# Optimization experiments

Measured on AMD Instinct MI355X. Metric: run time of the kernel, lower is better.

## Reference

```python
import jax, jax.numpy as jnp
import numpy as np

B, S, D, F, E, K = 2, 2048, 1024, 1024, 8, 2


def setup_inputs() -> dict:
    key = jax.random.key(0)
    kx, kg, k1, k3, k2 = jax.random.split(key, 5)
    # kaiming_uniform_(a=sqrt(5)) => Uniform(-1/sqrt(fan_in), 1/sqrt(fan_in))
    x = jax.random.normal(kx, (B, S, D), dtype=jnp.float32)
    gate_w = jax.random.uniform(kg, (E, D), jnp.float32, -1.0, 1.0) / np.sqrt(D)
    w1 = jax.random.uniform(k1, (E, F, D), jnp.float32, -1.0, 1.0) / np.sqrt(D)
    w3 = jax.random.uniform(k3, (E, F, D), jnp.float32, -1.0, 1.0) / np.sqrt(D)
    w2 = jax.random.uniform(k2, (E, D, F), jnp.float32, -1.0, 1.0) / np.sqrt(F)
    return {"x": x, "gate_w": gate_w, "w1": w1, "w3": w3, "w2": w2}


def reference(x, gate_w, w1, w3, w2):
    b, s, d = x.shape
    T = b * s
    xf = x.reshape(T, d)                      # [T, D]
    # ---- Gate: softmax scores, top-k selection, renormalized weights ----
    logits = xf @ gate_w.T                    # [T, E]
    probs = jax.nn.softmax(logits, axis=-1)
    topk_w, topk_idx = jax.lax.top_k(probs, K)            # [T, K]
    topk_w = topk_w / jnp.sum(topk_w, axis=-1, keepdims=True)
    # Dense per-token gate matrix [T, E]; zero for unselected experts, so the
    # weighted combine below is exactly sum_k w_k * expert_{idx_k}(x).
    gate_full = jnp.zeros((T, E), x.dtype).at[
        jnp.arange(T)[:, None], topk_idx].add(topk_w)
    # ---- Grouped SwiGLU experts: loop over small fixed E, vectorized over tokens ----
    out = jnp.zeros_like(xf)
    for e in range(E):
        h = jax.nn.silu(xf @ w1[e].T) * (xf @ w3[e].T)    # [T, F]
        out = out + gate_full[:, e:e + 1] * (h @ w2[e].T)  # [T, D]
    return out.reshape(b, s, d)
```

## Files before the change

### kernel.cpp

```cpp
#include <hip/hip_runtime.h>
#include <hip/hip_bf16.h>
#include <cstdint>
#include <cstddef>

#define T_TOK 4096
#define DDIM  1024
#define FDIM  1024
#define NEXP  8

typedef __attribute__((ext_vector_type(8))) short bf16x8;
typedef __attribute__((ext_vector_type(4))) float f32x4;
typedef __attribute__((ext_vector_type(8))) unsigned short u16x8;

__device__ __forceinline__ unsigned short f2bf(float f) {
  unsigned int u = __float_as_uint(f);
  u += 0x7FFFu + ((u >> 16) & 1u);
  return (unsigned short)(u >> 16);
}
__device__ __forceinline__ float bf2f(unsigned short u) {
  return __uint_as_float(((unsigned int)u) << 16);
}

__device__ __forceinline__ void gload_lds16(const void* g, void* l) {
  __builtin_amdgcn_global_load_lds(
      (const __attribute__((address_space(1))) unsigned int*)g,
      (__attribute__((address_space(3))) unsigned int*)l, 16, 0, 0);
}

__device__ __forceinline__ void vwait6() { asm volatile("s_waitcnt vmcnt(6)" ::: "memory"); }
__device__ __forceinline__ void vwait0() { asm volatile("s_waitcnt vmcnt(0)" ::: "memory"); }
__device__ __forceinline__ void lwait0() { asm volatile("s_waitcnt lgkmcnt(0)" ::: "memory"); }
__device__ __forceinline__ void barr()   { asm volatile("s_barrier" ::: "memory"); }

__device__ __forceinline__ bf16x8 frag_ld(const unsigned short* tile, int row, int kk) {
  int byteoff = (row << 7) + ((kk * 2) ^ ((row & 7) << 4));
  return *reinterpret_cast<const bf16x8*>(reinterpret_cast<const char*>(tile) + byteoff);
}

__global__ __launch_bounds__(256) void prep_kernel(
    const float* __restrict__ w1, const float* __restrict__ w3,
    unsigned short* __restrict__ W1b, unsigned short* __restrict__ W3b,
    const float* __restrict__ x, const float* __restrict__ gw,
    unsigned int* __restrict__ Xb32, int* __restrict__ tkidx, float* __restrict__ tkw,
    int* __restrict__ curp) {
  __shared__ float gws[NEXP * DDIM];
  const int bid = blockIdx.x;
  const int tid = threadIdx.x;

  if (bid < 2048) {
    const int sub = bid >> 10;
    const int b = bid & 1023;
    const float* s = (sub == 0) ? w1 : w3;
    unsigned short* d = (sub == 0) ? W1b : W3b;
    const int n = NEXP * FDIM * DDIM;
    const int stride = 1024 * 256 * 8;
    for (int i = (b * 256 + tid) * 8; i < n; i += stride) {
      float4 a = *reinterpret_cast<const float4*>(s + i);
      float4 c = *reinterpret_cast<const float4*>(s + i + 4);
      u16x8 o;
      o[0] = f2bf(a.x); o[1] = f2bf(a.y); o[2] = f2bf(a.z); o[3] = f2bf(a.w);
      o[4] = f2bf(c.x); o[5] = f2bf(c.y); o[6] = f2bf(c.z); o[7] = f2bf(c.w);
      *reinterpret_cast<u16x8*>(d + i) = o;
    }
    return;
  }

  const int lane = tid & 63;
  const int wid = tid >> 6;
  if (bid == 2048 && tid < NEXP) curp[tid * 32] = 0;
  for (int i = tid; i < NEXP * DDIM / 4; i += 256)
    reinterpret_cast<float4*>(gws)[i] = reinterpret_cast<const float4*>(gw)[i];
  __syncthreads();

  const int t = (bid - 2048) * 4 + wid;
  const float2* xr = reinterpret_cast<const float2*>(x + (size_t)t * DDIM);
  float2 xv[8];
#pragma unroll
  for (int i = 0; i < 8; ++i) xv[i] = xr[i * 64 + lane];
#pragma unroll
  for (int i = 0; i < 8; ++i)
    Xb32[(size_t)t * 512 + i * 64 + lane] =
        (unsigned int)f2bf(xv[i].x) | ((unsigned int)f2bf(xv[i].y) << 16);
  float p[NEXP];
#pragma unroll
  for (int e = 0; e < NEXP; ++e) p[e] = 0.f;
#pragma unroll
  for (int i = 0; i < 8; ++i) {
    const int k = (i * 64 + lane) * 2;
#pragma unroll
    for (int e = 0; e < NEXP; ++e)
      p[e] += xv[i].x * gws[e * DDIM + k] + xv[i].y * gws[e * DDIM + k + 1];
  }
#pragma unroll
  for (int s = 32; s > 0; s >>= 1)
#pragma unroll
    for (int e = 0; e < NEXP; ++e) p[e] += __shfl_xor(p[e], s, 64);
  if (lane == 0) {
    int i0 = 0; float l0 = p[0];
#pragma unroll
    for (int e = 1; e < NEXP; ++e) if (p[e] > l0) { l0 = p[e]; i0 = e; }
    int i1 = -1; float l1 = -1e30f;
#pragma unroll
    for (int e = 0; e < NEXP; ++e) if (e != i0 && p[e] > l1) { l1 = p[e]; i1 = e; }
    float ex = __expf(l1 - l0);
    float w0 = 1.f / (1.f + ex);
    float w1v = ex / (1.f + ex);
    tkidx[t * 2] = i0; tkidx[t * 2 + 1] = i1;
    tkw[t * 2] = w0;   tkw[t * 2 + 1] = w1v;
  }
}

__global__ __launch_bounds__(256) void fill_kernel(const int* __restrict__ tkidx,
                                                   const float* __restrict__ tkw,
                                                   int* __restrict__ offp,
                                                   int* __restrict__ curp,
                                                   int* __restrict__ list,
                                                   float* __restrict__ rgate,
                                                   int* __restrict__ wmap,
                                                   int* __restrict__ nwp) {
  __shared__ int ghist[4][NEXP];
  __shared__ int lhist[NEXP], base[NEXP];
  const int tid = threadIdx.x;
  if (tid < 32) ghist[tid >> 3][tid & 7] = 0;
  if (tid < NEXP) lhist[tid] = 0;
  __syncthreads();
  for (int i = tid; i < 2 * T_TOK; i += 256)
    atomicAdd(&ghist[tid >> 6][tkidx[i]], 1);
  const int t = blockIdx.x * 256 + tid;
  const int e0 = tkidx[t * 2], e1 = tkidx[t * 2 + 1];
  const int r0 = atomicAdd(&lhist[e0], 1);
  const int r1 = atomicAdd(&lhist[e1], 1);
  __syncthreads();
  if (blockIdx.x == 0 && tid == 64) {
    int nw = 0;
    for (int e = 0; e < NEXP; ++e) {
      int c = ghist[0][e] + ghist[1][e] + ghist[2][e] + ghist[3][e];
      int nrt = (c + 127) >> 7;
      for (int r = 0; r < nrt; ++r) wmap[nw++] = (e << 8) | r;
    }
    nwp[0] = nw;
  }
  if (tid < NEXP) {
    int o = 0;
#pragma unroll
    for (int j = 0; j < NEXP; ++j) {
      int c = ghist[0][j] + ghist[1][j] + ghist[2][j] + ghist[3][j];
      if (j < tid) o += c;
    }
    if (blockIdx.x == 0) {
      offp[tid] = o;
      if (tid == NEXP - 1)
        offp[NEXP] = o + ghist[0][tid] + ghist[1][tid] + ghist[2][tid] + ghist[3][tid];
    }
    base[tid] = o + atomicAdd(&curp[tid * 32], lhist[tid]);
  }
  __syncthreads();
  const int p0 = base[e0] + r0;
  const int p1 = base[e1] + r1;
  list[p0] = (t << 1);     rgate[p0] = tkw[t * 2];
  list[p1] = (t << 1) | 1; rgate[p1] = tkw[t * 2 + 1];
}

__global__ __launch_bounds__(256) void gemm1_kernel(
    const unsigned short* __restrict__ Xb, const unsigned short* __restrict__ W1b,
    const unsigned short* __restrict__ W3b, unsigned short* __restrict__ Hb,
    const int* __restrict__ off, const int* __restrict__ list,
    const int* __restrict__ wmap, const int* __restrict__ nwp,
    const float* __restrict__ w2, unsigned short* __restrict__ W2b) {
  const int bid0 = blockIdx.x;
  const int tid = threadIdx.x;

  if (bid0 >= 72 * 32) {
    const int b = bid0 - 72 * 32;
    const int n = NEXP * FDIM * DDIM;
    const int stride = 1024 * 256 * 8;
    for (int i = (b * 256 + tid) * 8; i < n; i += stride) {
      float4 a = *reinterpret_cast<const float4*>(w2 + i);
      float4 c = *reinterpret_cast<const float4*>(w2 + i + 4);
      u16x8 o;
      o[0] = f2bf(a.x); o[1] = f2bf(a.y); o[2] = f2bf(a.z); o[3] = f2bf(a.w);
      o[4] = f2bf(c.x); o[5] = f2bf(c.y); o[6] = f2bf(c.z); o[7] = f2bf(c.w);
      *reinterpret_cast<u16x8*>(W2b + i) = o;
    }
    return;
  }

  const int slot = bid0 >> 5;
  const int ft = bid0 & 31;
  if (slot >= nwp[0]) return;
  const int ent = wmap[slot];
  const int e = ent >> 8;
  const int rt = ent & 255;
  const int seg0 = off[e];
  const int Ne = off[e + 1] - seg0;
  const int rowbase = rt * 128;
  const int f0 = ft * 32;

  __shared__ unsigned short As[2][128 * 64];
  __shared__ unsigned short B1s[2][32 * 64];
  __shared__ unsigned short B3s[2][32 * 64];

  const int lane = tid & 63;
  const int wid = tid >> 6;
  const int wr = wid >> 1, wc = wid & 1;

  int ldsoffA[4]; size_t abase[4];
#pragma unroll
  for (int j = 0; j < 4; ++j) {
    int boff = j * 4096 + wid * 1024 + lane * 16;
    int row = boff >> 7;
    int c = ((boff >> 4) & 7) ^ (row & 7);
    ldsoffA[j] = (j * 4096 + wid * 1024) >> 1;
    int ar = rowbase + row; if (ar > Ne - 1) ar = Ne - 1;
    int tok = list[seg0 + ar] >> 1;
    abase[j] = (size_t)tok * DDIM + c * 8;
  }
  int ldsoffB; size_t bbase;
  {
    int boff = tid * 16;
    int row = boff >> 7;
    int c = ((boff >> 4) & 7) ^ (row & 7);
    ldsoffB = (wid * 1024) >> 1;
    bbase = (size_t)(e * FDIM + f0 + row) * DDIM + c * 8;
  }

  f32x4 acc1[4], acc3[4];
  const f32x4 z = {0.f, 0.f, 0.f, 0.f};
#pragma unroll
  for (int m = 0; m < 4; ++m) { acc1[m] = z; acc3[m] = z; }

  auto stage = [&](int buf, int kt) {
    const int ko = kt * 64;
#pragma unroll
    for (int j = 0; j < 4; ++j)
      gload_lds16(Xb + abase[j] + ko, &As[buf][ldsoffA[j]]);
    gload_lds16(W1b + bbase + ko, &B1s[buf][ldsoffB]);
    gload_lds16(W3b + bbase + ko, &B3s[buf][ldsoffB]);
  };

  const int lrow = lane & 15;
  const int kb = (lane >> 4) * 8;

  vwait0();
  stage(0, 0);
  stage(1, 1);
  vwait6();
  barr();

  for (int t = 0; t < 16; ++t) {
    const int b = t & 1;
#pragma unroll
    for (int ks = 0; ks < 2; ++ks) {
      bf16x8 a[4], p, q;
#pragma unroll
      for (int m = 0; m < 4; ++m)
        a[m] = frag_ld(As[b], wr * 64 + m * 16 + lrow, ks * 32 + kb);
      p = frag_ld(B1s[b], wc * 16 + lrow, ks * 32 + kb);
      q = frag_ld(B3s[b], wc * 16 + lrow, ks * 32 + kb);
#pragma unroll
      for (int m = 0; m < 4; ++m) {
        acc1[m] = __builtin_amdgcn_mfma_f32_16x16x32_bf16(a[m], p, acc1[m], 0, 0, 0);
        acc3[m] = __builtin_amdgcn_mfma_f32_16x16x32_bf16(a[m], q, acc3[m], 0, 0, 0);
      }
    }
    if (t == 15) break;
    lwait0();
    barr();
    if (t + 2 < 16) stage(b, t + 2);
    if (t < 14) vwait6(); else vwait0();
    barr();
  }

#pragma unroll
  for (int m = 0; m < 4; ++m)
#pragma unroll
    for (int r = 0; r < 4; ++r) {
      int rloc = wr * 64 + m * 16 + ((lane >> 4) << 2) + r;
      if (rowbase + rloc < Ne) {
        float v1 = acc1[m][r], v3 = acc3[m][r];
        float h = v1 / (1.f + __expf(-v1)) * v3;
        int col = f0 + wc * 16 + (lane & 15);
        Hb[(size_t)(seg0 + rowbase + rloc) * FDIM + col] = f2bf(h);
      }
    }
}

__global__ __launch_bounds__(256) void gemm2_kernel(
    const unsigned short* __restrict__ Hb, const unsigned short* __restrict__ W2b,
    unsigned short* __restrict__ Yb, const int* __restrict__ off,
    const int* __restrict__ list, const float* __restrict__ rgate,
    const int* __restrict__ wmap, const int* __restrict__ nwp) {
  const int bid0 = blockIdx.x;
  const int slot = bid0 >> 4;
  const int dt = bid0 & 15;
  if (slot >= nwp[0]) return;
  const int ent = wmap[slot];
  const int e = ent >> 8;
  const int rt = ent & 255;
  const int seg0 = off[e];
  const int Ne = off[e + 1] - seg0;
  const int rowbase = rt * 128;
  const int d0 = dt * 64;

  __shared__ unsigned short As[2][128 * 64];
  __shared__ unsigned short Bs[2][64 * 64];

  const int tid = threadIdx.x;
  const int lane = tid & 63;
  const int wid = tid >> 6;
  const int wr = wid >> 1, wc = wid & 1;

  int ldsoffA[4]; size_t abase[4];
  int ldsoffB[2]; size_t bbase[2];
#pragma unroll
  for (int j = 0; j < 4; ++j) {
    int boff = j * 4096 + wid * 1024 + lane * 16;
    int row = boff >> 7;
    int c = ((boff >> 4) & 7) ^ (row & 7);
    ldsoffA[j] = (j * 4096 + wid * 1024) >> 1;
    int ar = rowbase + row; if (ar > Ne - 1) ar = Ne - 1;
    abase[j] = (size_t)(seg0 + ar) * FDIM + c * 8;
  }
#pragma unroll
  for (int j = 0; j < 2; ++j) {
    int boff = j * 4096 + wid * 1024 + lane * 16;
    int row = boff >> 7;
    int c = ((boff >> 4) & 7) ^ (row & 7);
    ldsoffB[j] = (j * 4096 + wid * 1024) >> 1;
    bbase[j] = (size_t)(e * DDIM + d0 + row) * FDIM + c * 8;
  }

  f32x4 acc[4][2];
  const f32x4 z = {0.f, 0.f, 0.f, 0.f};
#pragma unroll
  for (int m = 0; m < 4; ++m)
#pragma unroll
    for (int n = 0; n < 2; ++n) acc[m][n] = z;

  auto stage = [&](int buf, int kt) {
    const int ko = kt * 64;
#pragma unroll
    for (int j = 0; j < 4; ++j)
      gload_lds16(Hb + abase[j] + ko, &As[buf][ldsoffA[j]]);
#pragma unroll
    for (int j = 0; j < 2; ++j)
      gload_lds16(W2b + bbase[j] + ko, &Bs[buf][ldsoffB[j]]);
  };

  const int lrow = lane & 15;
  const int kb = (lane >> 4) * 8;

  vwait0();
  stage(0, 0);
  stage(1, 1);
  vwait6();
  barr();

  for (int t = 0; t < 16; ++t) {
    const int b = t & 1;
#pragma unroll
    for (int ks = 0; ks < 2; ++ks) {
      bf16x8 a[4], bb[2];
#pragma unroll
      for (int m = 0; m < 4; ++m)
        a[m] = frag_ld(As[b], wr * 64 + m * 16 + lrow, ks * 32 + kb);
#pragma unroll
      for (int n = 0; n < 2; ++n)
        bb[n] = frag_ld(Bs[b], wc * 32 + n * 16 + lrow, ks * 32 + kb);
#pragma unroll
      for (int m = 0; m < 4; ++m)
#pragma unroll
        for (int n = 0; n < 2; ++n)
          acc[m][n] = __builtin_amdgcn_mfma_f32_16x16x32_bf16(a[m], bb[n], acc[m][n], 0, 0, 0);
    }
    if (t == 15) break;
    lwait0();
    barr();
    if (t + 2 < 16) stage(b, t + 2);
    if (t < 14) vwait6(); else vwait0();
    barr();
  }

#pragma unroll
  for (int m = 0; m < 4; ++m)
#pragma unroll
    for (int r = 0; r < 4; ++r) {
      int rloc = wr * 64 + m * 16 + ((lane >> 4) << 2) + r;
      if (rowbase + rloc < Ne) {
        int rg = seg0 + rowbase + rloc;
        int tk = list[rg];
        float gsc = rgate[rg];
#pragma unroll
        for (int n = 0; n < 2; ++n) {
          int col = d0 + wc * 32 + n * 16 + (lane & 15);
          Yb[(size_t)tk * DDIM + col] = f2bf(gsc * acc[m][n][r]);
        }
      }
    }
}

__global__ __launch_bounds__(256) void combine_kernel(const unsigned short* __restrict__ Yb,
                                                      float* __restrict__ out) {
  const int n = T_TOK * DDIM / 8;
  const int stride = gridDim.x * blockDim.x;
  for (int i = blockIdx.x * blockDim.x + threadIdx.x; i < n; i += stride) {
    int t = i >> 7;
    int c = (i & 127) * 8;
    u16x8 a = *reinterpret_cast<const u16x8*>(Yb + ((size_t)t * 2) * DDIM + c);
    u16x8 b = *reinterpret_cast<const u16x8*>(Yb + ((size_t)t * 2 + 1) * DDIM + c);
    float4 o0, o1;
    o0.x = bf2f(a[0]) + bf2f(b[0]); o0.y = bf2f(a[1]) + bf2f(b[1]);
    o0.z = bf2f(a[2]) + bf2f(b[2]); o0.w = bf2f(a[3]) + bf2f(b[3]);
    o1.x = bf2f(a[4]) + bf2f(b[4]); o1.y = bf2f(a[5]) + bf2f(b[5]);
    o1.z = bf2f(a[6]) + bf2f(b[6]); o1.w = bf2f(a[7]) + bf2f(b[7]);
    float* dst = out + (size_t)t * DDIM + c;
    *reinterpret_cast<float4*>(dst) = o0;
    *reinterpret_cast<float4*>(dst + 4) = o1;
  }
}

extern "C" void kernel_launch(void* const* d_in, const int* in_sizes, int n_in,
                              void* d_out, int out_size, void* d_ws, size_t ws_size,
                              hipStream_t stream) {
  (void)in_sizes; (void)n_in; (void)ws_size; (void)out_size;
  const float* x  = (const float*)d_in[0];
  const float* gw = (const float*)d_in[1];
  const float* w1 = (const float*)d_in[2];
  const float* w3 = (const float*)d_in[3];
  const float* w2 = (const float*)d_in[4];
  float* out = (float*)d_out;

  char* ws = (char*)d_ws;
  unsigned short* Xb  = (unsigned short*)(ws + 0);
  unsigned short* W1b = (unsigned short*)(ws + 8388608);
  unsigned short* W3b = (unsigned short*)(ws + 25165824);
  unsigned short* W2b = (unsigned short*)(ws + 41943040);
  unsigned short* Hb  = (unsigned short*)(ws + 58720256);
  unsigned short* Yb  = (unsigned short*)(ws + 8388608);
  int*   ctrl  = (int*)(ws + 75497472);
  int*   off   = ctrl;
  int*   nwp   = ctrl + 12;
  int*   curp  = ctrl + 16;
  int*   wmap  = ctrl + 256;
  int*   tkidx = (int*)(ws + 75497472 + 4096);
  float* tkw   = (float*)(ws + 75497472 + 4096 + 32768);
  int*   list  = (int*)(ws + 75497472 + 4096 + 65536);
  float* rgate = (float*)(ws + 75497472 + 4096 + 98304);

  prep_kernel<<<3072, 256, 0, stream>>>(w1, w3, W1b, W3b,
                                        x, gw, (unsigned int*)Xb, tkidx, tkw, curp);
  fill_kernel<<<16, 256, 0, stream>>>(tkidx, tkw, off, curp, list, rgate, wmap, nwp);

  gemm1_kernel<<<72 * 32 + 1024, 256, 0, stream>>>(Xb, W1b, W3b, Hb, off, list,
                                                   wmap, nwp, w2, W2b);
  gemm2_kernel<<<72 * 16, 256, 0, stream>>>(Hb, W2b, Yb, off, list, rgate, wmap, nwp);
  combine_kernel<<<2048, 256, 0, stream>>>(Yb, out);
}
```

Baseline: 132.9 us.

## Widen gemm1 F tile to 128 and drop double-buffered async pipeline

The gemm1 tile grows from 128x32 to 128x128 in F, so each block computes 4x4 MFMA sub-tiles per wave for both W1 and W3. This cuts the grid from 2304 to 576 compute blocks and reuses each A tile across four times more columns. The two-stage LDS pipeline with explicit vmcnt waits is replaced by a single-buffered load, syncthreads, compute, syncthreads loop. That exposes global load latency, and the accumulator count rises to 128 floats per thread, which adds register pressure and lowers occupancy.

```diff
diff --git a/kernel.cpp b/kernel.cpp
--- a/kernel.cpp
+++ b/kernel.cpp
@@ -170,8 +170,8 @@
   const int bid0 = blockIdx.x;
   const int tid = threadIdx.x;
 
-  if (bid0 >= 72 * 32) {
-    const int b = bid0 - 72 * 32;
+  if (bid0 >= 72 * 8) {
+    const int b = bid0 - 72 * 8;
     const int n = NEXP * FDIM * DDIM;
     const int stride = 1024 * 256 * 8;
     for (int i = (b * 256 + tid) * 8; i < n; i += stride) {
@@ -185,8 +185,8 @@
     return;
   }
 
-  const int slot = bid0 >> 5;
-  const int ft = bid0 & 31;
+  const int slot = bid0 >> 3;
+  const int ft = bid0 & 7;
   if (slot >= nwp[0]) return;
   const int ent = wmap[slot];
   const int e = ent >> 8;
@@ -194,81 +194,65 @@
   const int seg0 = off[e];
   const int Ne = off[e + 1] - seg0;
   const int rowbase = rt * 128;
-  const int f0 = ft * 32;
-
-  __shared__ unsigned short As[2][128 * 64];
-  __shared__ unsigned short B1s[2][32 * 64];
-  __shared__ unsigned short B3s[2][32 * 64];
+  const int f0 = ft * 128;
+
+  __shared__ unsigned short As[128 * 64];
+  __shared__ unsigned short B1s[128 * 64];
+  __shared__ unsigned short B3s[128 * 64];
 
   const int lane = tid & 63;
   const int wid = tid >> 6;
   const int wr = wid >> 1, wc = wid & 1;
 
-  int ldsoffA[4]; size_t abase[4];
+  int ldsoff[4]; size_t abase[4]; size_t bbase[4];
 #pragma unroll
   for (int j = 0; j < 4; ++j) {
     int boff = j * 4096 + wid * 1024 + lane * 16;
     int row = boff >> 7;
     int c = ((boff >> 4) & 7) ^ (row & 7);
-    ldsoffA[j] = (j * 4096 + wid * 1024) >> 1;
+    ldsoff[j] = (j * 4096 + wid * 1024) >> 1;
     int ar = rowbase + row; if (ar > Ne - 1) ar = Ne - 1;
     int tok = list[seg0 + ar] >> 1;
     abase[j] = (size_t)tok * DDIM + c * 8;
-  }
-  int ldsoffB; size_t bbase;
-  {
-    int boff = tid * 16;
-    int row = boff >> 7;
-    int c = ((boff >> 4) & 7) ^ (row & 7);
-    ldsoffB = (wid * 1024) >> 1;
-    bbase = (size_t)(e * FDIM + f0 + row) * DDIM + c * 8;
-  }
-
-  f32x4 acc1[4], acc3[4];
+    bbase[j] = (size_t)(e * FDIM + f0 + row) * DDIM + c * 8;
+  }
+
+  f32x4 acc1[4][4], acc3[4][4];
   const f32x4 z = {0.f, 0.f, 0.f, 0.f};
 #pragma unroll
-  for (int m = 0; m < 4; ++m) { acc1[m] = z; acc3[m] = z; }
-
-  auto stage = [&](int buf, int kt) {
-    const int ko = kt * 64;
-#pragma unroll
-    for (int j = 0; j < 4; ++j)
-      gload_lds16(Xb + abase[j] + ko, &As[buf][ldsoffA[j]]);
-    gload_lds16(W1b + bbase + ko, &B1s[buf][ldsoffB]);
-    gload_lds16(W3b + bbase + ko, &B3s[buf][ldsoffB]);
-  };
+  for (int m = 0; m < 4; ++m)
+#pragma unroll
+    for (int n = 0; n < 4; ++n) { acc1[m][n] = z; acc3[m][n] = z; }
 
   const int lrow = lane & 15;
   const int kb = (lane >> 4) * 8;
-
-  vwait0();
-  stage(0, 0);
-  stage(1, 1);
-  vwait6();
-  barr();
-
-  for (int t = 0; t < 16; ++t) {
-    const int b = t & 1;
+  for (int kt = 0; kt < DDIM / 64; ++kt) {
+    const int ko = kt * 64;
+#pragma unroll
+    for (int j = 0; j < 4; ++j) {
+      gload_lds16(Xb + abase[j] + ko, &As[ldsoff[j]]);
+      gload_lds16(W1b + bbase[j] + ko, &B1s[ldsoff[j]]);
+      gload_lds16(W3b + bbase[j] + ko, &B3s[ldsoff[j]]);
+    }
+    __syncthreads();
 #pragma unroll
     for (int ks = 0; ks < 2; ++ks) {
-      bf16x8 a[4], p, q;
+      bf16x8 a[4];
 #pragma unroll
       for (int m = 0; m < 4; ++m)
-        a[m] = frag_ld(As[b], wr * 64 + m * 16 + lrow, ks * 32 + kb);
-      p = frag_ld(B1s[b], wc * 16 + lrow, ks * 32 + kb);
-      q = frag_ld(B3s[b], wc * 16 + lrow, ks * 32 + kb);
-#pragma unroll
-      for (int m = 0; m < 4; ++m) {
-        acc1[m] = __builtin_amdgcn_mfma_f32_16x16x32_bf16(a[m], p, acc1[m], 0, 0, 0);
-        acc3[m] = __builtin_amdgcn_mfma_f32_16x16x32_bf16(a[m], q, acc3[m], 0, 0, 0);
+        a[m] = frag_ld(As, wr * 64 + m * 16 + lrow, ks * 32 + kb);
+#pragma unroll
+      for (int n = 0; n < 4; ++n) {
+        bf16x8 p = frag_ld(B1s, wc * 64 + n * 16 + lrow, ks * 32 + kb);
+        bf16x8 q = frag_ld(B3s, wc * 64 + n * 16 + lrow, ks * 32 + kb);
+#pragma unroll
+        for (int m = 0; m < 4; ++m) {
+          acc1[m][n] = __builtin_amdgcn_mfma_f32_16x16x32_bf16(a[m], p, acc1[m][n], 0, 0, 0);
+          acc3[m][n] = __builtin_amdgcn_mfma_f32_16x16x32_bf16(a[m], q, acc3[m][n], 0, 0, 0);
+        }
       }
     }
-    if (t == 15) break;
-    lwait0();
-    barr();
-    if (t + 2 < 16) stage(b, t + 2);
-    if (t < 14) vwait6(); else vwait0();
-    barr();
+    __syncthreads();
   }
 
 #pragma unroll
@@ -277,10 +261,13 @@
     for (int r = 0; r < 4; ++r) {
       int rloc = wr * 64 + m * 16 + ((lane >> 4) << 2) + r;
       if (rowbase + rloc < Ne) {
-        float v1 = acc1[m][r], v3 = acc3[m][r];
-        float h = v1 / (1.f + __expf(-v1)) * v3;
-        int col = f0 + wc * 16 + (lane & 15);
-        Hb[(size_t)(seg0 + rowbase + rloc) * FDIM + col] = f2bf(h);
+#pragma unroll
+        for (int n = 0; n < 4; ++n) {
+          float v1 = acc1[m][n][r], v3 = acc3[m][n][r];
+          float h = v1 / (1.f + __expf(-v1)) * v3;
+          int col = f0 + wc * 64 + n * 16 + (lane & 15);
+          Hb[(size_t)(seg0 + rowbase + rloc) * FDIM + col] = f2bf(h);
+        }
       }
     }
 }
@@ -451,8 +438,8 @@
                                         x, gw, (unsigned int*)Xb, tkidx, tkw, curp);
   fill_kernel<<<16, 256, 0, stream>>>(tkidx, tkw, off, curp, list, rgate, wmap, nwp);
 
-  gemm1_kernel<<<72 * 32 + 1024, 256, 0, stream>>>(Xb, W1b, W3b, Hb, off, list,
-                                                   wmap, nwp, w2, W2b);
+  gemm1_kernel<<<72 * 8 + 1024, 256, 0, stream>>>(Xb, W1b, W3b, Hb, off, list,
+                                                  wmap, nwp, w2, W2b);
   gemm2_kernel<<<72 * 16, 256, 0, stream>>>(Hb, W2b, Yb, off, list, rgate, wmap, nwp);
   combine_kernel<<<2048, 256, 0, stream>>>(Yb, out);
 }
```

After: 166.3 us. +25.1%, slower.
